# Kernel tuning notes

Measured on AMD Instinct MI355X. Metric: run time of the kernel, lower is better.

Reference implementation:

```python
import jax, jax.numpy as jnp
import numpy as np

N_NODES = 50000
N_EDGES = 800000
HIDDEN = 128
N_LAYERS = 3
N_MASKED = 25000
N_GRAPHS = 64


def setup_inputs() -> dict:
    key = jax.random.key(0)
    ks = jax.random.split(key, 8)
    scale = 1.0 / np.sqrt(HIDDEN)
    return {
        "x": jax.random.normal(ks[0], (N_NODES, HIDDEN), dtype=jnp.float32),
        "edge_index": jax.random.randint(ks[1], (2, N_EDGES), 0, N_NODES, dtype=jnp.int64),
        "mask": jax.random.randint(ks[2], (N_MASKED,), 0, N_NODES, dtype=jnp.int64),
        "batch": jnp.sort(jax.random.randint(ks[3], (N_MASKED,), 0, N_GRAPHS, dtype=jnp.int64)),
        "conv_w": jax.random.normal(ks[4], (N_LAYERS, HIDDEN, HIDDEN), dtype=jnp.float32) * scale,
        "conv_b": jnp.zeros((N_LAYERS, HIDDEN), dtype=jnp.float32),
        "lt1_w": jax.random.normal(ks[5], (HIDDEN,), dtype=jnp.float32) * scale,
        "lt1_b": jnp.zeros((1,), dtype=jnp.float32),
    }


def reference(x, edge_index, mask, batch, conv_w, conv_b, lt1_w, lt1_b):
    n = x.shape[0]
    # GCNConv: add self-loops, symmetric normalization D^-1/2 (A+I) D^-1/2
    loops = jnp.arange(n, dtype=edge_index.dtype)
    src = jnp.concatenate([edge_index[0], loops])
    dst = jnp.concatenate([edge_index[1], loops])
    deg = jax.ops.segment_sum(jnp.ones_like(src, dtype=x.dtype), dst, num_segments=n)
    dinv = jax.lax.rsqrt(deg)  # deg >= 1 because of self-loops
    norm = (dinv[src] * dinv[dst])[:, None]  # [E+N, 1]

    h = x
    for l in range(N_LAYERS):
        hw = h @ conv_w[l]                                  # [N, H]
        agg = jax.ops.segment_sum(hw[src] * norm, dst, num_segments=n)
        h = jax.nn.elu(agg + conv_b[l])                     # dropout is identity in eval mode

    xm = h[mask]                                            # [M, H] masked-node features
    pooled = jax.ops.segment_max(xm, batch, num_segments=N_GRAPHS)  # global_max_pool
    return pooled @ lt1_w[:, None] + lt1_b                  # [G, 1]
```

## Files before the change

kernel.cpp:

```cpp
#include <hip/hip_runtime.h>
#include <math.h>

#define N_NODES  50000
#define N_EDGES  800000
#define HIDDEN   128
#define N_LAYERS 3
#define N_MASKED 25000
#define N_GRAPHS 64
#define XSLICE   6250
#define EPB      8192
#define NCHUNK   ((N_EDGES + EPB - 1) / EPB)

typedef __attribute__((ext_vector_type(8))) short bf16x8;
typedef __attribute__((ext_vector_type(4))) float f32x4;

__device__ __forceinline__ unsigned fmap(float f) {
    unsigned u = __float_as_uint(f);
    return (u & 0x80000000u) ? ~u : (u | 0x80000000u);
}
__device__ __forceinline__ float funmap(unsigned u) {
    return __uint_as_float((u & 0x80000000u) ? (u & 0x7FFFFFFFu) : ~u);
}

__device__ __forceinline__ unsigned pack_split(float x) {
    unsigned u = __float_as_uint(x);
    unsigned hi = (u + 0x7fffu + ((u >> 16) & 1u)) >> 16;
    float rem = x - __uint_as_float(hi << 16);
    unsigned v = __float_as_uint(rem);
    unsigned lo = (v + 0x7fffu + ((v >> 16) & 1u)) >> 16;
    return hi | (lo << 16);
}

__global__ void count_deg_kernel(const int* __restrict__ dst, unsigned* __restrict__ deg) {
    const int xcd = blockIdx.x & 7;
    const int chunk = blockIdx.x >> 3;
    const int lo = xcd * XSLICE, hi = lo + XSLICE;
    const int base = chunk * EPB;
    const int end = (base + EPB < N_EDGES) ? base + EPB : N_EDGES;
    for (int e = base + threadIdx.x * 4; e < end; e += 256 * 4) {
        int4 d4 = *(const int4*)(dst + e);
        if (d4.x >= lo && d4.x < hi) atomicAdd(&deg[d4.x], 1u);
        if (d4.y >= lo && d4.y < hi) atomicAdd(&deg[d4.y], 1u);
        if (d4.z >= lo && d4.z < hi) atomicAdd(&deg[d4.z], 1u);
        if (d4.w >= lo && d4.w < hi) atomicAdd(&deg[d4.w], 1u);
    }
}

__global__ void scan_block_kernel(const unsigned* __restrict__ deg, unsigned* __restrict__ incl,
                                  unsigned* __restrict__ bsum) {
    __shared__ unsigned s[1024];
    int i = blockIdx.x * 1024 + threadIdx.x;
    unsigned v = (i < N_NODES) ? deg[i] : 0u;
    s[threadIdx.x] = v;
    __syncthreads();
    for (int off = 1; off < 1024; off <<= 1) {
        unsigned t = (threadIdx.x >= off) ? s[threadIdx.x - off] : 0u;
        __syncthreads();
        s[threadIdx.x] += t;
        __syncthreads();
    }
    if (i < N_NODES) incl[i] = s[threadIdx.x];
    if (threadIdx.x == 1023) bsum[blockIdx.x] = s[1023];
}

__global__ void scan_bsum_kernel(unsigned* __restrict__ bsum, int n) {
    int lane = threadIdx.x;
    unsigned v = (lane < n) ? bsum[lane] : 0u;
    #pragma unroll
    for (int off = 1; off < 64; off <<= 1) {
        unsigned t = __shfl_up(v, off);
        if (lane >= off) v += t;
    }
    unsigned ex = __shfl_up(v, 1);
    if (lane == 0) ex = 0u;
    if (lane < n) bsum[lane] = ex;
}

__global__ void scan_finalize_kernel(const unsigned* __restrict__ incl,
                                     const unsigned* __restrict__ bsum_ex,
                                     const unsigned* __restrict__ deg,
                                     unsigned* __restrict__ row_ptr,
                                     unsigned* __restrict__ cursor,
                                     float* __restrict__ dinv) {
    int i = blockIdx.x * blockDim.x + threadIdx.x;
    if (i <= N_NODES) {
        unsigned v = (i == 0) ? 0u : incl[i - 1] + bsum_ex[(i - 1) >> 10];
        row_ptr[i] = v;
        if (i < N_NODES) {
            cursor[(size_t)i << 4] = v;
            dinv[i] = rsqrtf((float)(deg[i] + 1u));
        }
    }
}

__global__ void fill_csr_kernel(const int* __restrict__ src, const int* __restrict__ dst,
                                unsigned* __restrict__ cursor, int* __restrict__ csr_src) {
    const int xcd = blockIdx.x & 7;
    const int chunk = blockIdx.x >> 3;
    const int lo = xcd * XSLICE, hi = lo + XSLICE;
    const int base = chunk * EPB;
    const int end = (base + EPB < N_EDGES) ? base + EPB : N_EDGES;
    for (int e = base + threadIdx.x * 4; e < end; e += 256 * 4) {
        int4 d4 = *(const int4*)(dst + e);
        int4 s4 = *(const int4*)(src + e);
        if (d4.x >= lo && d4.x < hi) csr_src[atomicAdd(&cursor[(size_t)d4.x << 4], 1u)] = s4.x;
        if (d4.y >= lo && d4.y < hi) csr_src[atomicAdd(&cursor[(size_t)d4.y << 4], 1u)] = s4.y;
        if (d4.z >= lo && d4.z < hi) csr_src[atomicAdd(&cursor[(size_t)d4.z << 4], 1u)] = s4.z;
        if (d4.w >= lo && d4.w < hi) csr_src[atomicAdd(&cursor[(size_t)d4.w << 4], 1u)] = s4.w;
    }
}

__global__ void wprep_kernel(const float* __restrict__ W,
                             unsigned short* __restrict__ Whi,
                             unsigned short* __restrict__ Wlo) {
    int idx = blockIdx.x * 256 + threadIdx.x;
    if (idx >= 3 * 16384) return;
    int j     = idx & 7;
    int lane  = (idx >> 3) & 63;
    int ct    = (idx >> 9) & 7;
    int ks    = (idx >> 12) & 3;
    int layer = idx >> 14;
    int k = ks * 32 + (lane >> 4) * 8 + j;
    int n = ct * 16 + (lane & 15);
    unsigned p = pack_split(W[layer * 16384 + k * 128 + n]);
    Whi[idx] = (unsigned short)(p & 0xffffu);
    Wlo[idx] = (unsigned short)(p >> 16);
}

template<int MODE, int AMODE>
__global__ __launch_bounds__(512, 1) void mfma_gemm_kernel(const unsigned* __restrict__ Aval,
                                                           const unsigned short* __restrict__ Wh,
                                                           const unsigned short* __restrict__ Wl,
                                                           const float* __restrict__ dinv,
                                                           const float* __restrict__ bias,
                                                           const int* __restrict__ batch,
                                                           unsigned* __restrict__ gmax,
                                                           float* __restrict__ Out,
                                                           int nrows) {
    extern __shared__ char smem[];
    unsigned short* WhL = (unsigned short*)smem;
    unsigned short* WlL = (unsigned short*)(smem + 32768);
    uint4* AL4 = (uint4*)(smem + 65536);
    const int tid = threadIdx.x;
    const int lane = tid & 63;
    const int w = tid >> 6;

    {
        const uint4* gh = (const uint4*)Wh;
        const uint4* gl = (const uint4*)Wl;
        uint4* sh = (uint4*)WhL;
        uint4* sl = (uint4*)WlL;
        #pragma unroll
        for (int i = 0; i < 4; ++i) {
            sh[tid + i * 512] = gh[tid + i * 512];
            sl[tid + i * 512] = gl[tid + i * 512];
        }
    }

    const int ntiles = (nrows + 127) >> 7;
    const int rloc = w * 16 + (lane & 15);
    const int rx = rloc & 7;
    const int colBase = lane & 15;
    const int rgrp = lane >> 4;

    for (int t = blockIdx.x; t < ntiles; t += gridDim.x) {
        const int tileBase = t * 128;
        __syncthreads();

        #pragma unroll
        for (int i = 0; i < 8; ++i) {
            int n = tid + i * 512;
            int r = n >> 5;
            int c16 = n & 31;
            int grow = tileBase + r;
            if (grow > nrows - 1) grow = nrows - 1;
            uint4 v = *(const uint4*)(Aval + (size_t)grow * 128 + c16 * 4);
            if (AMODE == 1) {
                v.x = pack_split(__uint_as_float(v.x));
                v.y = pack_split(__uint_as_float(v.y));
                v.z = pack_split(__uint_as_float(v.z));
                v.w = pack_split(__uint_as_float(v.w));
            }
            AL4[r * 32 + (c16 ^ (r & 7))] = v;
        }
        __syncthreads();

        f32x4 acc[8];
        #pragma unroll
        for (int c = 0; c < 8; ++c) acc[c] = (f32x4){0.f, 0.f, 0.f, 0.f};

        #pragma unroll
        for (int ks = 0; ks < 4; ++ks) {
            int c0 = ks * 8 + (lane >> 4) * 2;
            uint4 a0 = AL4[rloc * 32 + (c0 ^ rx)];
            uint4 a1 = AL4[rloc * 32 + ((c0 + 1) ^ rx)];
            unsigned pv[8] = {a0.x, a0.y, a0.z, a0.w, a1.x, a1.y, a1.z, a1.w};
            bf16x8 ah, al;
            #pragma unroll
            for (int j = 0; j < 8; ++j) {
                ah[j] = (short)(pv[j] & 0xffffu);
                al[j] = (short)(pv[j] >> 16);
            }
            const unsigned short* wbh = WhL + ks * 4096 + lane * 8;
            const unsigned short* wbl = WlL + ks * 4096 + lane * 8;
            #pragma unroll
            for (int ct = 0; ct < 8; ++ct) {
                bf16x8 bh = *(const bf16x8*)(wbh + ct * 512);
                bf16x8 bl = *(const bf16x8*)(wbl + ct * 512);
                acc[ct] = __builtin_amdgcn_mfma_f32_16x16x32_bf16(ah, bh, acc[ct], 0, 0, 0);
                acc[ct] = __builtin_amdgcn_mfma_f32_16x16x32_bf16(al, bh, acc[ct], 0, 0, 0);
                acc[ct] = __builtin_amdgcn_mfma_f32_16x16x32_bf16(ah, bl, acc[ct], 0, 0, 0);
            }
        }

        #pragma unroll
        for (int r = 0; r < 4; ++r) {
            int row = tileBase + w * 16 + rgrp * 4 + r;
            if (row >= nrows) continue;
            float d = 0.f;
            int bofs = 0;
            if (MODE == 0 || MODE == 1) d = dinv[row];
            if (MODE == 2) bofs = batch[row] * 128;
            #pragma unroll
            for (int ct = 0; ct < 8; ++ct) {
                int col = ct * 16 + colBase;
                float o = acc[ct][r];
                if (MODE == 0) {
                    Out[(size_t)row * 128 + col] = o * d;
                } else {
                    o += bias[col];
                    o = o > 0.f ? o : expm1f(o);
                    if (MODE == 1) Out[(size_t)row * 128 + col] = o * d;
                    else           atomicMax(&gmax[bofs + col], fmap(o));
                }
            }
        }
    }
}

template<int GMODE>
__global__ __launch_bounds__(256) void gather_kernel(const float* __restrict__ tab,
                                                     const unsigned* __restrict__ row_ptr,
                                                     const int* __restrict__ csr_src,
                                                     const float* __restrict__ dinv,
                                                     const float* __restrict__ bias,
                                                     float* __restrict__ outf,
                                                     unsigned* __restrict__ outp,
                                                     const int* __restrict__ nodes,
                                                     int n_items) {
    int wid = (blockIdx.x * blockDim.x + threadIdx.x) >> 6;
    int w = wid >> 1;
    if (w >= n_items) return;
    const int f = ((wid & 1) << 6) | (threadIdx.x & 63);
    const int v = nodes ? nodes[w] : w;

    const unsigned s0 = row_ptr[v], e0 = row_ptr[v + 1];
    const float* __restrict__ base = tab + f;

    float acc[8];
    #pragma unroll
    for (int j = 0; j < 8; ++j) acc[j] = 0.f;
    acc[0] = base[(size_t)v << 7];

    unsigned i = s0;
    if (i + 8 <= e0) {
        int idx[8];
        #pragma unroll
        for (int j = 0; j < 8; ++j) idx[j] = csr_src[i + j];
        for (; i + 16 <= e0; i += 8) {
            int nxt[8];
            #pragma unroll
            for (int j = 0; j < 8; ++j) nxt[j] = csr_src[i + 8 + j];
            #pragma unroll
            for (int j = 0; j < 8; ++j) acc[j] += base[(size_t)idx[j] << 7];
            #pragma unroll
            for (int j = 0; j < 8; ++j) idx[j] = nxt[j];
        }
        #pragma unroll
        for (int j = 0; j < 8; ++j) acc[j] += base[(size_t)idx[j] << 7];
        i += 8;
    }
    if (i + 4 <= e0) {
        #pragma unroll
        for (int j = 0; j < 4; ++j) acc[j] += base[(size_t)csr_src[i + j] << 7];
        i += 4;
    }
    for (; i < e0; ++i) acc[0] += base[(size_t)csr_src[i] << 7];

    float dv = dinv[v];
    float sumall = ((acc[0] + acc[1]) + (acc[2] + acc[3])) +
                   ((acc[4] + acc[5]) + (acc[6] + acc[7]));
    if (GMODE == 0) {
        float o = dv * sumall + bias[f];
        o = o > 0.f ? o : expm1f(o);
        outf[((size_t)w << 7) + f] = o * dv;
    } else {
        outp[((size_t)w << 7) + f] = pack_split(dv * sumall);
    }
}

__global__ void gmax_init_kernel(unsigned* __restrict__ gmax) {
    int i = blockIdx.x * blockDim.x + threadIdx.x;
    if (i < N_GRAPHS * 128) gmax[i] = 0x007FFFFFu;
}

__global__ void pool_finish_kernel(const unsigned* __restrict__ gmax,
                                   const float* __restrict__ w, const float* __restrict__ b,
                                   float* __restrict__ out) {
    const int g = blockIdx.x;
    const int f = threadIdx.x;
    float val = funmap(gmax[g * 128 + f]) * w[f];
    #pragma unroll
    for (int off = 32; off > 0; off >>= 1) val += __shfl_down(val, off);
    __shared__ float ps[2];
    if ((threadIdx.x & 63) == 0) ps[threadIdx.x >> 6] = val;
    __syncthreads();
    if (threadIdx.x == 0) out[g] = ps[0] + ps[1] + b[0];
}

extern "C" void kernel_launch(void* const* d_in, const int* in_sizes, int n_in,
                              void* d_out, int out_size, void* d_ws, size_t ws_size,
                              hipStream_t stream) {
    const float* x      = (const float*)d_in[0];
    const int*   ei     = (const int*)d_in[1];
    const int*   mask   = (const int*)d_in[2];
    const int*   batch  = (const int*)d_in[3];
    const float* conv_w = (const float*)d_in[4];
    const float* conv_b = (const float*)d_in[5];
    const float* lt1_w  = (const float*)d_in[6];
    const float* lt1_b  = (const float*)d_in[7];
    float* out = (float*)d_out;

    const int* e_src = ei;
    const int* e_dst = ei + N_EDGES;

    char* ws = (char*)d_ws;
    auto carve = [&](size_t bytes) { char* p = ws; ws += (bytes + 255) & ~(size_t)255; return p; };
    unsigned* deg     = (unsigned*)carve(N_NODES * 4);
    float*    dinv    = (float*)   carve(N_NODES * 4);
    unsigned* row_ptr = (unsigned*)carve((N_NODES + 1) * 4);
    unsigned* cursor  = (unsigned*)carve((size_t)N_NODES * 64);
    unsigned* bsum    = (unsigned*)carve(64 * 4);
    unsigned* gmax    = (unsigned*)carve(N_GRAPHS * 128 * 4);
    unsigned short* wph = (unsigned short*)carve(3 * 16384 * 2);
    unsigned short* wpl = (unsigned short*)carve(3 * 16384 * 2);
    int*      csr_src = (int*)     carve((size_t)N_EDGES * 4);
    char*     reg1    = carve((size_t)N_NODES * HIDDEN * 4);
    char*     reg2    = carve((size_t)N_NODES * HIDDEN * 4);
    unsigned* incl    = (unsigned*)csr_src;

    float*    bufB  = (float*)reg1;
    float*    bufB2 = (float*)reg1;
    float*    bufA  = (float*)reg2;
    unsigned* bufAp = (unsigned*)reg2;
    unsigned* bufCp = (unsigned*)reg2;

    const int NB_SCAN = (N_NODES + 1023) / 1024;

    hipMemsetAsync(deg, 0, N_NODES * sizeof(unsigned), stream);
    count_deg_kernel<<<8 * NCHUNK, 256, 0, stream>>>(e_dst, deg);
    scan_block_kernel<<<NB_SCAN, 1024, 0, stream>>>(deg, incl, bsum);
    scan_bsum_kernel<<<1, 64, 0, stream>>>(bsum, NB_SCAN);
    scan_finalize_kernel<<<(N_NODES + 256) / 256, 256, 0, stream>>>(incl, bsum, deg,
                                                                    row_ptr, cursor, dinv);
    fill_csr_kernel<<<8 * NCHUNK, 256, 0, stream>>>(e_src, e_dst, cursor, csr_src);
    gmax_init_kernel<<<(N_GRAPHS * 128 + 255) / 256, 256, 0, stream>>>(gmax);
    wprep_kernel<<<(3 * 16384 + 255) / 256, 256, 0, stream>>>(conv_w, wph, wpl);

    const size_t LDS_BYTES = 131072;
    auto gemm_grid = [](int rows) { int t = (rows + 127) / 128; return t < 256 ? t : 256; };
    auto ga_blocks = [](int items) { return (items * 2 * 64 + 255) / 256; };

    mfma_gemm_kernel<0, 1><<<gemm_grid(N_NODES), 512, LDS_BYTES, stream>>>(
        (const unsigned*)x, wph, wpl, dinv, nullptr, nullptr, nullptr, bufA, N_NODES);
    gather_kernel<0><<<ga_blocks(N_NODES), 256, 0, stream>>>(
        bufA, row_ptr, csr_src, dinv, conv_b, bufB, nullptr, nullptr, N_NODES);
    gather_kernel<1><<<ga_blocks(N_NODES), 256, 0, stream>>>(
        bufB, row_ptr, csr_src, dinv, nullptr, nullptr, bufAp, nullptr, N_NODES);
    mfma_gemm_kernel<1, 0><<<gemm_grid(N_NODES), 512, LDS_BYTES, stream>>>(
        bufAp, wph + 16384, wpl + 16384, dinv, conv_b + HIDDEN, nullptr, nullptr,
        bufB2, N_NODES);
    gather_kernel<1><<<ga_blocks(N_MASKED), 256, 0, stream>>>(
        bufB2, row_ptr, csr_src, dinv, nullptr, nullptr, bufCp, mask, N_MASKED);
    mfma_gemm_kernel<2, 0><<<gemm_grid(N_MASKED), 512, LDS_BYTES, stream>>>(
        bufCp, wph + 32768, wpl + 32768, nullptr, conv_b + 2 * HIDDEN, batch, gmax,
        nullptr, N_MASKED);

    pool_finish_kernel<<<N_GRAPHS, HIDDEN, 0, stream>>>(gmax, lt1_w, lt1_b, out);
}
```

Baseline: 355.9 us.

## Use direct global-to-LDS loads in GEMM, prepack x, merge init kernels

The GEMM kernel now stages its weight and A tiles with direct global-to-LDS async loads (global_load_lds) instead of register round-trips, with the XOR swizzle applied on the global address side. To allow this, the fp32-to-split-bf16 packing of x moves out of the first GEMM into a separate xpack pass that writes a packed copy of x. The deg memset, gmax init and weight prep are merged into one init kernel to cut launches. The extra pass adds a full read and write of x, and the async loads depend on the barrier correctly waiting for LDS-destined loads.

```diff
diff --git a/kernel.cpp b/kernel.cpp
--- a/kernel.cpp
+++ b/kernel.cpp
@@ -14,6 +14,10 @@
 typedef __attribute__((ext_vector_type(8))) short bf16x8;
 typedef __attribute__((ext_vector_type(4))) float f32x4;
 
+#define GLOAD_LDS16(g, l) \
+    __builtin_amdgcn_global_load_lds((const __attribute__((address_space(1))) void*)(g), \
+                                     (__attribute__((address_space(3))) void*)(l), 16, 0, 0)
+
 __device__ __forceinline__ unsigned fmap(float f) {
     unsigned u = __float_as_uint(f);
     return (u & 0x80000000u) ? ~u : (u | 0x80000000u);
@@ -29,6 +33,39 @@
     unsigned v = __float_as_uint(rem);
     unsigned lo = (v + 0x7fffu + ((v >> 16) & 1u)) >> 16;
     return hi | (lo << 16);
+}
+
+__global__ void init_kernel(unsigned* __restrict__ deg, unsigned* __restrict__ gmax,
+                            const float* __restrict__ W,
+                            unsigned short* __restrict__ Whi,
+                            unsigned short* __restrict__ Wlo) {
+    const int b = blockIdx.x;
+    if (b < 196) {
+        int i = b * 256 + threadIdx.x;
+        if (i < N_NODES) deg[i] = 0u;
+    } else if (b < 228) {
+        int i = (b - 196) * 256 + threadIdx.x;
+        if (i < N_GRAPHS * 128) gmax[i] = 0x007FFFFFu;
+    } else {
+        int idx = (b - 228) * 256 + threadIdx.x;
+        if (idx < 3 * 16384) {
+            int j     = idx & 7;
+            int lane  = (idx >> 3) & 63;
+            int ct    = (idx >> 9) & 7;
+            int ks    = (idx >> 12) & 3;
+            int layer = idx >> 14;
+            int k = ks * 32 + (lane >> 4) * 8 + j;
+            int n = ct * 16 + (lane & 15);
+            unsigned p = pack_split(W[layer * 16384 + k * 128 + n]);
+            Whi[idx] = (unsigned short)(p & 0xffffu);
+            Wlo[idx] = (unsigned short)(p >> 16);
+        }
+    }
+}
+
+__global__ void xpack_kernel(const float* __restrict__ x, unsigned* __restrict__ xp, int n) {
+    int i = blockIdx.x * 256 + threadIdx.x;
+    if (i < n) xp[i] = pack_split(x[i]);
 }
 
 __global__ void count_deg_kernel(const int* __restrict__ dst, unsigned* __restrict__ deg) {
@@ -110,25 +147,8 @@
     }
 }
 
-__global__ void wprep_kernel(const float* __restrict__ W,
-                             unsigned short* __restrict__ Whi,
-                             unsigned short* __restrict__ Wlo) {
-    int idx = blockIdx.x * 256 + threadIdx.x;
-    if (idx >= 3 * 16384) return;
-    int j     = idx & 7;
-    int lane  = (idx >> 3) & 63;
-    int ct    = (idx >> 9) & 7;
-    int ks    = (idx >> 12) & 3;
-    int layer = idx >> 14;
-    int k = ks * 32 + (lane >> 4) * 8 + j;
-    int n = ct * 16 + (lane & 15);
-    unsigned p = pack_split(W[layer * 16384 + k * 128 + n]);
-    Whi[idx] = (unsigned short)(p & 0xffffu);
-    Wlo[idx] = (unsigned short)(p >> 16);
-}
-
-template<int MODE, int AMODE>
-__global__ __launch_bounds__(512, 1) void mfma_gemm_kernel(const unsigned* __restrict__ Aval,
+template<int MODE>
+__global__ __launch_bounds__(512, 1) void mfma_gemm_kernel(const unsigned* __restrict__ Ap,
                                                            const unsigned short* __restrict__ Wh,
                                                            const unsigned short* __restrict__ Wl,
                                                            const float* __restrict__ dinv,
@@ -145,16 +165,11 @@
     const int lane = tid & 63;
     const int w = tid >> 6;
 
-    {
-        const uint4* gh = (const uint4*)Wh;
-        const uint4* gl = (const uint4*)Wl;
-        uint4* sh = (uint4*)WhL;
-        uint4* sl = (uint4*)WlL;
-        #pragma unroll
-        for (int i = 0; i < 4; ++i) {
-            sh[tid + i * 512] = gh[tid + i * 512];
-            sl[tid + i * 512] = gl[tid + i * 512];
-        }
+    #pragma unroll
+    for (int i = 0; i < 4; ++i) {
+        int m = tid + i * 512;
+        GLOAD_LDS16((const char*)Wh + (size_t)m * 16, smem + (size_t)m * 16);
+        GLOAD_LDS16((const char*)Wl + (size_t)m * 16, smem + 32768 + (size_t)m * 16);
     }
 
     const int ntiles = (nrows + 127) >> 7;
@@ -171,17 +186,11 @@
         for (int i = 0; i < 8; ++i) {
             int n = tid + i * 512;
             int r = n >> 5;
-            int c16 = n & 31;
+            int c = n & 31;
             int grow = tileBase + r;
             if (grow > nrows - 1) grow = nrows - 1;
-            uint4 v = *(const uint4*)(Aval + (size_t)grow * 128 + c16 * 4);
-            if (AMODE == 1) {
-                v.x = pack_split(__uint_as_float(v.x));
-                v.y = pack_split(__uint_as_float(v.y));
-                v.z = pack_split(__uint_as_float(v.z));
-                v.w = pack_split(__uint_as_float(v.w));
-            }
-            AL4[r * 32 + (c16 ^ (r & 7))] = v;
+            GLOAD_LDS16(Ap + (size_t)grow * 128 + ((c ^ (r & 7)) << 2),
+                        smem + 65536 + (size_t)n * 16);
         }
         __syncthreads();
 
@@ -299,11 +308,6 @@
     }
 }
 
-__global__ void gmax_init_kernel(unsigned* __restrict__ gmax) {
-    int i = blockIdx.x * blockDim.x + threadIdx.x;
-    if (i < N_GRAPHS * 128) gmax[i] = 0x007FFFFFu;
-}
-
 __global__ void pool_finish_kernel(const unsigned* __restrict__ gmax,
                                    const float* __restrict__ w, const float* __restrict__ b,
                                    float* __restrict__ out) {
@@ -345,6 +349,7 @@
     unsigned short* wph = (unsigned short*)carve(3 * 16384 * 2);
     unsigned short* wpl = (unsigned short*)carve(3 * 16384 * 2);
     int*      csr_src = (int*)     carve((size_t)N_EDGES * 4);
+    unsigned* xp      = (unsigned*)carve((size_t)N_NODES * HIDDEN * 4);
     char*     reg1    = carve((size_t)N_NODES * HIDDEN * 4);
     char*     reg2    = carve((size_t)N_NODES * HIDDEN * 4);
     unsigned* incl    = (unsigned*)csr_src;
@@ -357,32 +362,31 @@
 
     const int NB_SCAN = (N_NODES + 1023) / 1024;
 
-    hipMemsetAsync(deg, 0, N_NODES * sizeof(unsigned), stream);
+    init_kernel<<<420, 256, 0, stream>>>(deg, gmax, conv_w, wph, wpl);
+    xpack_kernel<<<(N_NODES * HIDDEN + 255) / 256, 256, 0, stream>>>(x, xp, N_NODES * HIDDEN);
     count_deg_kernel<<<8 * NCHUNK, 256, 0, stream>>>(e_dst, deg);
     scan_block_kernel<<<NB_SCAN, 1024, 0, stream>>>(deg, incl, bsum);
     scan_bsum_kernel<<<1, 64, 0, stream>>>(bsum, NB_SCAN);
     scan_finalize_kernel<<<(N_NODES + 256) / 256, 256, 0, stream>>>(incl, bsum, deg,
                                                                     row_ptr, cursor, dinv);
     fill_csr_kernel<<<8 * NCHUNK, 256, 0, stream>>>(e_src, e_dst, cursor, csr_src);
-    gmax_init_kernel<<<(N_GRAPHS * 128 + 255) / 256, 256, 0, stream>>>(gmax);
-    wprep_kernel<<<(3 * 16384 + 255) / 256, 256, 0, stream>>>(conv_w, wph, wpl);
 
     const size_t LDS_BYTES = 131072;
     auto gemm_grid = [](int rows) { int t = (rows + 127) / 128; return t < 256 ? t : 256; };
     auto ga_blocks = [](int items) { return (items * 2 * 64 + 255) / 256; };
 
-    mfma_gemm_kernel<0, 1><<<gemm_grid(N_NODES), 512, LDS_BYTES, stream>>>(
-        (const unsigned*)x, wph, wpl, dinv, nullptr, nullptr, nullptr, bufA, N_NODES);
+    mfma_gemm_kernel<0><<<gemm_grid(N_NODES), 512, LDS_BYTES, stream>>>(
+        xp, wph, wpl, dinv, nullptr, nullptr, nullptr, bufA, N_NODES);
     gather_kernel<0><<<ga_blocks(N_NODES), 256, 0, stream>>>(
         bufA, row_ptr, csr_src, dinv, conv_b, bufB, nullptr, nullptr, N_NODES);
     gather_kernel<1><<<ga_blocks(N_NODES), 256, 0, stream>>>(
         bufB, row_ptr, csr_src, dinv, nullptr, nullptr, bufAp, nullptr, N_NODES);
-    mfma_gemm_kernel<1, 0><<<gemm_grid(N_NODES), 512, LDS_BYTES, stream>>>(
+    mfma_gemm_kernel<1><<<gemm_grid(N_NODES), 512, LDS_BYTES, stream>>>(
         bufAp, wph + 16384, wpl + 16384, dinv, conv_b + HIDDEN, nullptr, nullptr,
         bufB2, N_NODES);
     gather_kernel<1><<<ga_blocks(N_MASKED), 256, 0, stream>>>(
         bufB2, row_ptr, csr_src, dinv, nullptr, nullptr, bufCp, mask, N_MASKED);
-    mfma_gemm_kernel<2, 0><<<gemm_grid(N_MASKED), 512, LDS_BYTES, stream>>>(
+    mfma_gemm_kernel<2><<<gemm_grid(N_MASKED), 512, LDS_BYTES, stream>>>(
         bufCp, wph + 32768, wpl + 32768, nullptr, conv_b + 2 * HIDDEN, batch, gmax,
         nullptr, N_MASKED);
 
```

New measurement: 362.1 us. Within noise of the previous version (+1.7%).
